# Kernel tuning notes

Measured on AMD Instinct MI355X. Metric: run time of the kernel, lower is better.

Reference implementation:

```python
import jax, jax.numpy as jnp
import numpy as np
from jax import lax

N_HEADS = 8
KERNEL = 3
PAD = 1
D_MODEL = 512

def setup_inputs() -> dict:
    key = jax.random.key(0)
    k1, k2, k3 = jax.random.split(key, 3)
    x = jax.random.normal(k1, (64, 1024, D_MODEL), dtype=jnp.float32)
    weight = jax.random.normal(k2, (N_HEADS, 1, KERNEL), dtype=jnp.float32)
    fc_w = jax.random.normal(k3, (D_MODEL, D_MODEL), dtype=jnp.float32) * (1.0 / np.sqrt(D_MODEL))
    return {"x": x, "weight": weight, "fc_w": fc_w}

def reference(x, weight, fc_w):
    bs, gs, d_model = x.shape
    # weight_softmax=True: normalize kernel taps per head
    w = jax.nn.softmax(weight, axis=-1)  # [H, 1, K]
    # view(-1, n_heads, d_model): channels = heads, spatial axis = d_model
    x2 = x.reshape(-1, N_HEADS, d_model)  # [bs*gs/H, H, d_model]
    out = lax.conv_general_dilated(
        x2, w,
        window_strides=(1,),
        padding=[(PAD, PAD)],
        feature_group_count=N_HEADS,
        dimension_numbers=("NCH", "OIH", "NCH"),
    )  # depthwise conv along d_model
    out = out.reshape(bs, gs, d_model)
    # nn.Linear without bias: y = out @ fc_w.T
    return jnp.einsum("bgd,ed->bge", out, fc_w)
```

## Files before the change

kernel.cpp:

```cpp
#include <hip/hip_runtime.h>

typedef __attribute__((ext_vector_type(8))) __bf16  bf16x8;
typedef __attribute__((ext_vector_type(8))) short   short8;
typedef __attribute__((ext_vector_type(4))) float   f32x4;

#define DM   512
#define BM   128
#define BN   128
#define BK   32
#define NNT  4
#define NKT  16
#define TILEB (BN*BK*2)

__device__ __forceinline__ short f2bf(float f) {
  union { float f; unsigned u; } v; v.f = f;
  unsigned r = v.u + 0x7fffu + ((v.u >> 16) & 1u);
  return (short)(r >> 16);
}

__device__ __forceinline__ int slotA(int r, int s) {
  return (r >> 3) * 512 + (((r & 7) + (s << 3)) << 4);
}

__global__ void build_g_kernel(const float* __restrict__ w,
                               const float* __restrict__ fcw,
                               short* __restrict__ Gt) {
  int idx = blockIdx.x * 256 + threadIdx.x;
  int h  = idx >> 15;
  int t  = idx & 32767;
  int e  = t >> 6;
  int d0 = (t & 63) << 3;
  float w0 = w[h*3+0], w1 = w[h*3+1], w2 = w[h*3+2];
  float mx = fmaxf(w0, fmaxf(w1, w2));
  float e0 = __expf(w0-mx), e1 = __expf(w1-mx), e2 = __expf(w2-mx);
  float inv = 1.0f / (e0 + e1 + e2);
  float w0n = e0*inv, w1n = e1*inv, w2n = e2*inv;
  const float* row = fcw + e * DM;
  float v[10];
  v[0] = (d0 > 0) ? row[d0-1] : 0.0f;
  float4 a = *(const float4*)(row + d0);
  float4 b = *(const float4*)(row + d0 + 4);
  v[1]=a.x; v[2]=a.y; v[3]=a.z; v[4]=a.w;
  v[5]=b.x; v[6]=b.y; v[7]=b.z; v[8]=b.w;
  v[9] = (d0 + 8 < DM) ? row[d0+8] : 0.0f;
  short8 sv;
  #pragma unroll
  for (int j = 0; j < 8; ++j)
    sv[j] = f2bf(w1n*v[j+1] + w0n*v[j+2] + w2n*v[j]);
  int nt = e >> 7, r = e & 127;
  int kt = d0 >> 5;
  int s  = (d0 >> 3) & 3;
  char* tile = (char*)Gt + (size_t)((h * NNT + nt) * NKT + kt) * TILEB;
  *(short8*)(tile + slotA(r, s)) = sv;
}

__global__ __launch_bounds__(256, 4) void gemm_kernel(const float* __restrict__ x,
                                                      const short* __restrict__ Gt,
                                                      float* __restrict__ out) {
  int bid = blockIdx.x;
  int h   = bid & 7;
  int idx = bid >> 3;
  int nt  = idx & 3;
  int mt  = idx >> 2;
  int tid  = threadIdx.x;
  int lane = tid & 63;
  int wid  = tid >> 6;
  int wr = wid >> 1, wc = wid & 1;
  int ln = lane & 15, sf = lane >> 4;

  __shared__ short Alds[2][BM * BK];
  __shared__ short Blds[2][BN * BK];

  const char* Bsrc0 = (const char*)Gt + (size_t)(h * NNT + nt) * NKT * TILEB;
  const float* Abase = x + (size_t)(h + 8 * (size_t)mt * BM) * DM;

  float4 ap[4];

  auto loadA = [&](int kt) {
    #pragma unroll
    for (int p = 0; p < 2; ++p) {
      int r = (tid >> 2) + 64 * p;
      const float* xr = Abase + (size_t)r * 8 * DM + kt * BK + (tid & 3) * 8;
      ap[2*p]   = *(const float4*)xr;
      ap[2*p+1] = *(const float4*)(xr + 4);
    }
  };
  auto stageB = [&](int kt, int buf) {
    const char* src = Bsrc0 + kt * TILEB;
    char* dst = (char*)Blds[buf];
    #pragma unroll
    for (int p = 0; p < 2; ++p)
      __builtin_amdgcn_global_load_lds((const void*)(src + p * 4096 + tid * 16),
                                       (void*)(dst + p * 4096 + wid * 1024), 16, 0, 0);
  };
  auto writeA = [&](int buf) {
    char* dst = (char*)Alds[buf];
    #pragma unroll
    for (int p = 0; p < 2; ++p) {
      int r = (tid >> 2) + 64 * p;
      bf16x8 v;
      v[0]=(__bf16)ap[2*p].x;   v[1]=(__bf16)ap[2*p].y;
      v[2]=(__bf16)ap[2*p].z;   v[3]=(__bf16)ap[2*p].w;
      v[4]=(__bf16)ap[2*p+1].x; v[5]=(__bf16)ap[2*p+1].y;
      v[6]=(__bf16)ap[2*p+1].z; v[7]=(__bf16)ap[2*p+1].w;
      *(bf16x8*)(dst + slotA(r, tid & 3)) = v;
    }
  };

  f32x4 acc[4][4] = {};

  auto computeTile = [&](int cur) {
    const char* Ap = (const char*)Alds[cur];
    const char* Bp = (const char*)Blds[cur];
    bf16x8 af[4], bfr[4];
    #pragma unroll
    for (int m = 0; m < 4; ++m)
      af[m] = *(const bf16x8*)(Ap + slotA(wr*64 + m*16 + ln, sf));
    #pragma unroll
    for (int n = 0; n < 4; ++n)
      bfr[n] = *(const bf16x8*)(Bp + slotA(wc*64 + n*16 + ln, sf));
    #pragma unroll
    for (int m = 0; m < 4; ++m)
      #pragma unroll
      for (int n = 0; n < 4; ++n)
        acc[m][n] = __builtin_amdgcn_mfma_f32_16x16x32_bf16(af[m], bfr[n], acc[m][n], 0, 0, 0);
  };

  loadA(0);
  stageB(0, 0);
  writeA(0);
  __syncthreads();

  for (int kt = 0; kt < NKT; ++kt) {
    int cur = kt & 1, nxt = cur ^ 1;
    if (kt + 1 < NKT) {
      loadA(kt + 1);
      stageB(kt + 1, nxt);
    }
    computeTile(cur);
    if (kt + 1 < NKT) writeA(nxt);
    __syncthreads();
  }

  int e0 = nt * BN + wc * 64 + ln;
  #pragma unroll
  for (int m = 0; m < 4; ++m) {
    int tq = mt * BM + wr * 64 + m * 16 + (sf << 2);
    #pragma unroll
    for (int j = 0; j < 4; ++j) {
      int R = h + 8 * (tq + j);
      float* orow = out + (size_t)R * DM + e0;
      #pragma unroll
      for (int n = 0; n < 4; ++n)
        orow[n * 16] = acc[m][n][j];
    }
  }
}

extern "C" void kernel_launch(void* const* d_in, const int* in_sizes, int n_in,
                              void* d_out, int out_size, void* d_ws, size_t ws_size,
                              hipStream_t stream) {
  const float* x   = (const float*)d_in[0];
  const float* w   = (const float*)d_in[1];
  const float* fcw = (const float*)d_in[2];
  float* out = (float*)d_out;
  short* Gt  = (short*)d_ws;

  hipLaunchKernelGGL(build_g_kernel, dim3((8 * DM * DM / 8) / 256), dim3(256), 0, stream,
                     w, fcw, Gt);
  hipLaunchKernelGGL(gemm_kernel, dim3(8 * 64 * NNT), dim3(256), 0, stream,
                     x, Gt, out);
}
```

Before: 85.44 us.

## Pre-convert x to bf16 tiled image and triple-buffer direct-to-LDS GEMM loads

Adds a pre-pass kernel that converts x to bf16 and writes it in an MFMA-ready tiled layout in workspace. The GEMM can then stream both A and B tiles with global_load_lds into a 3-stage LDS ring, using manual vmcnt waits and barriers. It also changes the LDS slot layout so each wave reads contiguous 1KB fragments. The aim is to halve A read bandwidth in the GEMM and remove the register round trip for A. The cost is an extra kernel launch plus a full write and reread of the bf16 copy of x. A fallback path is kept for when the workspace is too small.

```diff
diff --git a/kernel.cpp b/kernel.cpp
--- a/kernel.cpp
+++ b/kernel.cpp
@@ -10,16 +10,20 @@
 #define BK   32
 #define NNT  4
 #define NKT  16
-#define TILEB (BN*BK*2)
+#define TILEB 8192
+#define NMT  64
+#define G_BYTES   (8 * NNT * NKT * TILEB)
+#define A_BYTES   (8 * NMT * NKT * TILEB)
+#define WS_NEED   (G_BYTES + A_BYTES)
+
+__device__ __forceinline__ int idoff(int r, int s) {
+  return (r >> 4) * 1024 + (((r & 15) + (s << 4)) << 4);
+}
 
 __device__ __forceinline__ short f2bf(float f) {
   union { float f; unsigned u; } v; v.f = f;
   unsigned r = v.u + 0x7fffu + ((v.u >> 16) & 1u);
   return (short)(r >> 16);
-}
-
-__device__ __forceinline__ int slotA(int r, int s) {
-  return (r >> 3) * 512 + (((r & 7) + (s << 3)) << 4);
 }
 
 __global__ void build_g_kernel(const float* __restrict__ w,
@@ -47,16 +51,128 @@
   #pragma unroll
   for (int j = 0; j < 8; ++j)
     sv[j] = f2bf(w1n*v[j+1] + w0n*v[j+2] + w2n*v[j]);
-  int nt = e >> 7, r = e & 127;
-  int kt = d0 >> 5;
-  int s  = (d0 >> 3) & 3;
+  int nt = e >> 7, er = e & 127;
+  int kt = d0 >> 5, s = (d0 >> 3) & 3;
   char* tile = (char*)Gt + (size_t)((h * NNT + nt) * NKT + kt) * TILEB;
-  *(short8*)(tile + slotA(r, s)) = sv;
-}
-
-__global__ __launch_bounds__(256, 4) void gemm_kernel(const float* __restrict__ x,
-                                                      const short* __restrict__ Gt,
-                                                      float* __restrict__ out) {
+  *(short8*)(tile + idoff(er, s)) = sv;
+}
+
+__global__ __launch_bounds__(256) void build_a_kernel(const float* __restrict__ x,
+                                                      char* __restrict__ Aimg) {
+  int bid = blockIdx.x;
+  int kt = bid & 15;
+  int mt = (bid >> 4) & 63;
+  int h  = bid >> 10;
+  int tid = threadIdx.x;
+  char* tile = Aimg + (size_t)bid * TILEB;
+  #pragma unroll
+  for (int p = 0; p < 2; ++p) {
+    int r = (tid >> 2) + 64 * p;
+    int s = tid & 3;
+    const float* xr = x + (size_t)(h + 8 * (mt * 128 + r)) * DM + kt * BK + s * 8;
+    float4 va = *(const float4*)xr;
+    float4 vb = *(const float4*)(xr + 4);
+    bf16x8 v;
+    v[0]=(__bf16)va.x; v[1]=(__bf16)va.y; v[2]=(__bf16)va.z; v[3]=(__bf16)va.w;
+    v[4]=(__bf16)vb.x; v[5]=(__bf16)vb.y; v[6]=(__bf16)vb.z; v[7]=(__bf16)vb.w;
+    *(bf16x8*)(tile + idoff(r, s)) = v;
+  }
+}
+
+__global__ __launch_bounds__(256, 4) void gemm_img(const char* __restrict__ Aimg,
+                                                   const char* __restrict__ Gt,
+                                                   float* __restrict__ out) {
+  int bid = blockIdx.x;
+  int h   = bid & 7;
+  int idx = bid >> 3;
+  int nt  = idx & 3;
+  int mt  = idx >> 2;
+  int tid  = threadIdx.x;
+  int lane = tid & 63;
+  int wid  = tid >> 6;
+  int wr = wid >> 1, wc = wid & 1;
+
+  __shared__ char Abuf[3 * TILEB];
+  __shared__ char Bbuf[3 * TILEB];
+
+  const char* Asrc0 = Aimg + (size_t)((h * NMT + mt) * NKT) * TILEB;
+  const char* Bsrc0 = Gt + (size_t)((h * NNT + nt) * NKT) * TILEB;
+
+  f32x4 acc[4][4] = {};
+
+#define STAGE(KT, BUF) do {                                                  \
+    const char* as_ = Asrc0 + (KT) * TILEB;                                  \
+    const char* bs_ = Bsrc0 + (KT) * TILEB;                                  \
+    char* ad_ = Abuf + (BUF) * TILEB;                                        \
+    char* bd_ = Bbuf + (BUF) * TILEB;                                        \
+    _Pragma("unroll")                                                        \
+    for (int p = 0; p < 2; ++p) {                                            \
+      __builtin_amdgcn_global_load_lds((const void*)(as_ + p*4096 + tid*16), \
+                                       (void*)(ad_ + p*4096 + wid*1024), 16, 0, 0); \
+      __builtin_amdgcn_global_load_lds((const void*)(bs_ + p*4096 + tid*16), \
+                                       (void*)(bd_ + p*4096 + wid*1024), 16, 0, 0); \
+    }                                                                        \
+  } while (0)
+
+#define COMP(BUF) do {                                                       \
+    const char* Ap_ = Abuf + (BUF) * TILEB;                                  \
+    const char* Bp_ = Bbuf + (BUF) * TILEB;                                  \
+    bf16x8 af[4], bfr[4];                                                    \
+    _Pragma("unroll")                                                        \
+    for (int m = 0; m < 4; ++m)                                              \
+      af[m] = *(const bf16x8*)(Ap_ + (wr*4 + m)*1024 + lane*16);             \
+    _Pragma("unroll")                                                        \
+    for (int n = 0; n < 4; ++n)                                              \
+      bfr[n] = *(const bf16x8*)(Bp_ + (wc*4 + n)*1024 + lane*16);            \
+    _Pragma("unroll")                                                        \
+    for (int m = 0; m < 4; ++m)                                              \
+      _Pragma("unroll")                                                      \
+      for (int n = 0; n < 4; ++n)                                            \
+        acc[m][n] = __builtin_amdgcn_mfma_f32_16x16x32_bf16(af[m], bfr[n],   \
+                                                            acc[m][n], 0,0,0);\
+  } while (0)
+
+#define BND4() do { asm volatile("s_waitcnt vmcnt(4)" ::: "memory");         \
+    __builtin_amdgcn_sched_barrier(0); __builtin_amdgcn_s_barrier();         \
+    __builtin_amdgcn_sched_barrier(0); } while (0)
+#define BND0() do { asm volatile("s_waitcnt vmcnt(0)" ::: "memory");         \
+    __builtin_amdgcn_sched_barrier(0); __builtin_amdgcn_s_barrier();         \
+    __builtin_amdgcn_sched_barrier(0); } while (0)
+
+#define GI(T)  do { STAGE((T)+2, ((T)+2)%3); COMP((T)%3); BND4(); } while (0)
+
+  STAGE(0, 0); STAGE(1, 1);
+  BND4();
+  GI(0);  GI(1);  GI(2);  GI(3);  GI(4);  GI(5);  GI(6);
+  GI(7);  GI(8);  GI(9);  GI(10); GI(11); GI(12); GI(13);
+  COMP(14 % 3); BND0();
+  COMP(15 % 3);
+
+#undef GI
+#undef BND4
+#undef BND0
+#undef COMP
+#undef STAGE
+
+  int ln = lane & 15, sf = lane >> 4;
+  int e0 = nt * BN + wc * 64 + ln;
+  #pragma unroll
+  for (int m = 0; m < 4; ++m) {
+    int tq = mt * BM + wr * 64 + m * 16 + (sf << 2);
+    #pragma unroll
+    for (int j = 0; j < 4; ++j) {
+      int R = h + 8 * (tq + j);
+      float* orow = out + (size_t)R * DM + e0;
+      #pragma unroll
+      for (int n = 0; n < 4; ++n)
+        orow[n * 16] = acc[m][n][j];
+    }
+  }
+}
+
+__global__ __launch_bounds__(256, 4) void gemm_fb(const float* __restrict__ x,
+                                                  const char* __restrict__ Gt,
+                                                  float* __restrict__ out) {
   int bid = blockIdx.x;
   int h   = bid & 7;
   int idx = bid >> 3;
@@ -68,14 +184,13 @@
   int wr = wid >> 1, wc = wid & 1;
   int ln = lane & 15, sf = lane >> 4;
 
-  __shared__ short Alds[2][BM * BK];
-  __shared__ short Blds[2][BN * BK];
-
-  const char* Bsrc0 = (const char*)Gt + (size_t)(h * NNT + nt) * NKT * TILEB;
+  __shared__ char Abuf[2 * TILEB];
+  __shared__ char Bbuf[2 * TILEB];
+
+  const char* Bsrc0 = Gt + (size_t)((h * NNT + nt) * NKT) * TILEB;
   const float* Abase = x + (size_t)(h + 8 * (size_t)mt * BM) * DM;
 
   float4 ap[4];
-
   auto loadA = [&](int kt) {
     #pragma unroll
     for (int p = 0; p < 2; ++p) {
@@ -87,14 +202,14 @@
   };
   auto stageB = [&](int kt, int buf) {
     const char* src = Bsrc0 + kt * TILEB;
-    char* dst = (char*)Blds[buf];
+    char* dst = Bbuf + buf * TILEB;
     #pragma unroll
     for (int p = 0; p < 2; ++p)
-      __builtin_amdgcn_global_load_lds((const void*)(src + p * 4096 + tid * 16),
-                                       (void*)(dst + p * 4096 + wid * 1024), 16, 0, 0);
+      __builtin_amdgcn_global_load_lds((const void*)(src + p*4096 + tid*16),
+                                       (void*)(dst + p*4096 + wid*1024), 16, 0, 0);
   };
   auto writeA = [&](int buf) {
-    char* dst = (char*)Alds[buf];
+    char* dst = Abuf + buf * TILEB;
     #pragma unroll
     for (int p = 0; p < 2; ++p) {
       int r = (tid >> 2) + 64 * p;
@@ -103,22 +218,21 @@
       v[2]=(__bf16)ap[2*p].z;   v[3]=(__bf16)ap[2*p].w;
       v[4]=(__bf16)ap[2*p+1].x; v[5]=(__bf16)ap[2*p+1].y;
       v[6]=(__bf16)ap[2*p+1].z; v[7]=(__bf16)ap[2*p+1].w;
-      *(bf16x8*)(dst + slotA(r, tid & 3)) = v;
+      *(bf16x8*)(dst + idoff(r, tid & 3)) = v;
     }
   };
 
   f32x4 acc[4][4] = {};
-
   auto computeTile = [&](int cur) {
-    const char* Ap = (const char*)Alds[cur];
-    const char* Bp = (const char*)Blds[cur];
+    const char* Ap = Abuf + cur * TILEB;
+    const char* Bp = Bbuf + cur * TILEB;
     bf16x8 af[4], bfr[4];
     #pragma unroll
     for (int m = 0; m < 4; ++m)
-      af[m] = *(const bf16x8*)(Ap + slotA(wr*64 + m*16 + ln, sf));
+      af[m] = *(const bf16x8*)(Ap + (wr*4 + m)*1024 + lane*16);
     #pragma unroll
     for (int n = 0; n < 4; ++n)
-      bfr[n] = *(const bf16x8*)(Bp + slotA(wc*64 + n*16 + ln, sf));
+      bfr[n] = *(const bf16x8*)(Bp + (wc*4 + n)*1024 + lane*16);
     #pragma unroll
     for (int m = 0; m < 4; ++m)
       #pragma unroll
@@ -126,17 +240,11 @@
         acc[m][n] = __builtin_amdgcn_mfma_f32_16x16x32_bf16(af[m], bfr[n], acc[m][n], 0, 0, 0);
   };
 
-  loadA(0);
-  stageB(0, 0);
-  writeA(0);
+  loadA(0); stageB(0, 0); writeA(0);
   __syncthreads();
-
   for (int kt = 0; kt < NKT; ++kt) {
     int cur = kt & 1, nxt = cur ^ 1;
-    if (kt + 1 < NKT) {
-      loadA(kt + 1);
-      stageB(kt + 1, nxt);
-    }
+    if (kt + 1 < NKT) { loadA(kt + 1); stageB(kt + 1, nxt); }
     computeTile(cur);
     if (kt + 1 < NKT) writeA(nxt);
     __syncthreads();
@@ -166,8 +274,16 @@
   float* out = (float*)d_out;
   short* Gt  = (short*)d_ws;
 
-  hipLaunchKernelGGL(build_g_kernel, dim3((8 * DM * DM / 8) / 256), dim3(256), 0, stream,
-                     w, fcw, Gt);
-  hipLaunchKernelGGL(gemm_kernel, dim3(8 * 64 * NNT), dim3(256), 0, stream,
-                     x, Gt, out);
-}
+  hipLaunchKernelGGL(build_g_kernel, dim3(1024), dim3(256), 0, stream, w, fcw, Gt);
+
+  if (ws_size >= (size_t)WS_NEED) {
+    char* Aimg = (char*)d_ws + G_BYTES;
+    hipLaunchKernelGGL(build_a_kernel, dim3(8 * NMT * NKT), dim3(256), 0, stream,
+                       x, Aimg);
+    hipLaunchKernelGGL(gemm_img, dim3(8 * NMT * NNT), dim3(256), 0, stream,
+                       Aimg, (const char*)Gt, out);
+  } else {
+    hipLaunchKernelGGL(gemm_fb, dim3(8 * NMT * NNT), dim3(256), 0, stream,
+                       x, (const char*)Gt, out);
+  }
+}
```

Result: slower. 103.8 us (+21.5%).
